# Performance work log

Hardware: AMD Instinct MI355X
Metric: run time of the kernel (lower is better)

Reference implementation:

```python
import jax, jax.numpy as jnp
import numpy as np

B, Q, C, H, NSTEPS = 1024, 96, 16, 100, 100  # batch, q (MA order), channels, hidden, Euler steps


def setup_inputs() -> dict:
    key = jax.random.key(0)
    ks = jax.random.split(key, 6)
    s = 0.1  # weight init scale
    return {
        "series": jax.random.normal(ks[0], (B, Q, C), jnp.float32),
        "rand_error": jax.random.normal(ks[1], (B, 1, C), jnp.float32),
        "W1": jax.random.normal(ks[2], (H, Q + 2), jnp.float32) * s,
        "b1": jnp.zeros((H,), jnp.float32),
        "W2": jax.random.normal(ks[3], (H, H), jnp.float32) * s,
        "b2": jnp.zeros((H,), jnp.float32),
        "W3": jax.random.normal(ks[4], (Q + 1, H), jnp.float32) * s,
        "b3": jnp.zeros((Q + 1,), jnp.float32),
    }


def _mlp(x, t, W1, b1, W2, b2, W3, b3):
    # x: (B, Q+1, C), t: (B, 1, C)  -> cat along feature dim, permute to (B, C, Q+2)
    inp = jnp.concatenate([x, t], axis=1).transpose(0, 2, 1)
    h = jnp.tanh(inp @ W1.T + b1)
    h = jnp.tanh(h @ W2.T + b2)
    out = h @ W3.T + b3            # (B, C, Q+1)
    return out.transpose(0, 2, 1)  # (B, Q+1, C)


def reference(series, rand_error, W1, b1, W2, b2, W3, b3):
    # ma_forecast sampling path: noise = cat(series, rand_error) then Euler flow sampling
    noise = jnp.concatenate([series, rand_error], axis=1)  # (B, Q+1, C)
    dt = jnp.float32(1.0 / NSTEPS)

    def step(x, i):
        t = jnp.ones((x.shape[0], 1, x.shape[2]), x.dtype) * (i.astype(x.dtype) / NSTEPS)
        pred = _mlp(x, t, W1, b1, W2, b2, W3, b3)
        return x + (pred - noise) * dt, None

    x, _ = jax.lax.scan(step, noise, jnp.arange(NSTEPS))
    return x
```

## Files before the change

### kernel.cpp

```cpp
#include <hip/hip_runtime.h>


#define NB 1024
#define NQ 96
#define NC 16
#define NH 100
#define QP1 97
#define QP2 98
#define NTHR 256
#define STR 136
#define NSTEPS_ 100
#define MT_K 128

typedef __attribute__((ext_vector_type(8))) short bf16x8;
typedef __attribute__((ext_vector_type(4))) short shortx4;
typedef __attribute__((ext_vector_type(4))) float f32x4;
typedef __attribute__((ext_vector_type(2))) float f32x2;
typedef __attribute__((ext_vector_type(4))) unsigned uintx4;

#define LO2(v) __builtin_shufflevector(v, v, 0, 1)
#define HI2(v) __builtin_shufflevector(v, v, 2, 3)

__device__ __forceinline__ f32x4 splat4(float f) {
  f32x4 v = f;
  return v;
}

__device__ __forceinline__ f32x2 splat2(float f) {
  f32x2 v = f;
  return v;
}

__device__ __forceinline__ short f2bf_rne(float f) {
  unsigned u = __builtin_bit_cast(unsigned, f);
  u = u + 0x7fffu + ((u >> 16) & 1u);
  return (short)(u >> 16);
}

__device__ __forceinline__ unsigned cvtpk_bf16(float a, float b) {
  unsigned r;
  asm("v_cvt_pk_bf16_f32 %0, %1, %2" : "=v"(r) : "v"(a), "v"(b));
  return r;
}

#if __has_builtin(__builtin_amdgcn_exp2f)
__device__ __forceinline__ float hexp2(float x) {
  return __builtin_amdgcn_exp2f(x);
}
#else
__device__ __forceinline__ float hexp2(float x) {
  float r;
  asm("v_exp_f32 %0, %1\n\ts_nop 1" : "=v"(r) : "v"(x));
  return r;
}
#endif

__device__ __forceinline__ float tanh1(float x) {
  float t = hexp2(x * 2.885390081777927f);
  float r = __builtin_amdgcn_rcpf(t + 1.0f);
  return fmaf(-2.0f, r, 1.0f);
}

__device__ __forceinline__ void tanh_pair(f32x2& p, f32x2& q) {
  p[0] = tanh1(p[0]);
  p[1] = tanh1(p[1]);
  q[0] = tanh1(q[0]);
  q[1] = tanh1(q[1]);
}

__global__ void __launch_bounds__(512) arima_prep(
    const float* __restrict__ W1, const float* __restrict__ b1,
    const float* __restrict__ W3, const float* __restrict__ b3,
    short* __restrict__ Mt, float* __restrict__ sv) {
  __shared__ float part[4][128];
  __shared__ float pb[128];
  const int n = blockIdx.x;
  const int tid = threadIdx.x;
  const int k = tid & 127, js = tid >> 7;
  float s = 0.0f;
  if (n < NH && k < NH) {
    int j0 = js * 25, j1 = (js == 3) ? QP1 : j0 + 25;
    for (int j = j0; j < j1; ++j)
      s = fmaf(W1[n * QP2 + j], W3[j * NH + k], s);
  }
  part[js][k] = s;
  if (tid < 128)
    pb[tid] = (tid < QP1 && n < NH) ? W1[n * QP2 + tid] * b3[tid] : 0.0f;
  __syncthreads();
  if (js == 0) {
    float tot = part[0][k] + part[1][k] + part[2][k] + part[3][k];
    Mt[n * MT_K + k] = f2bf_rne(0.01f * tot);
  }
  if (tid == 0) {
    float d = 0.0f;
    for (int j = 0; j < 128; ++j) d += pb[j];
    sv[n] = (n < NH) ? 0.01f * (d + b1[n] + W1[n * QP2 + QP1]) : 0.0f;
  }
}

__device__ void load_afrag(const float* __restrict__ W,
                           const float* __restrict__ bias, int ws, int mvalid,
                           int KW, int m, int quad, bf16x8 dst[4]) {
#pragma unroll
  for (int kb = 0; kb < 4; ++kb) {
    bf16x8 v;
#pragma unroll
    for (int i = 0; i < 8; ++i) {
      int kcol = kb * 32 + ((i >> 2) << 4) + quad * 4 + (i & 3);
      float f = 0.0f;
      if (m < mvalid) {
        if (kcol < KW) f = W[m * ws + kcol];
        else if (kcol == KW) f = bias[m];
      }
      v[i] = f2bf_rne(f);
    }
    dst[kb] = v;
  }
}

__device__ __forceinline__ void gemm_acc(const short* __restrict__ src,
                                         int rbase, const bf16x8 (&A)[2][4],
                                         f32x4 (&acc)[2]) {
#pragma unroll
  for (int kb = 0; kb < 4; ++kb) {
    bf16x8 bv = *(const bf16x8*)(src + rbase + kb * 32);
    acc[0] = __builtin_amdgcn_mfma_f32_16x16x32_bf16(A[0][kb], bv, acc[0], 0, 0, 0);
    acc[1] = __builtin_amdgcn_mfma_f32_16x16x32_bf16(A[1][kb], bv, acc[1], 0, 0, 0);
  }
}

__device__ __forceinline__ void write_tile(short* __restrict__ dst, int wrow,
                                           int T0, int quad, f32x2 a0,
                                           f32x2 a1, f32x2 b0, f32x2 b1) {
  uintx4 u;
  u.x = cvtpk_bf16(a0[0], a0[1]);
  u.y = cvtpk_bf16(a1[0], a1[1]);
  u.z = cvtpk_bf16(b0[0], b0[1]);
  u.w = cvtpk_bf16(b1[0], b1[1]);
  *(uintx4*)(dst + wrow + (T0 >> 1) * 32 + quad * 8) = u;
}

__global__ void __launch_bounds__(NTHR, 4)
arima_r20(const float* __restrict__ series,
          const float* __restrict__ rand_error, const float* __restrict__ W1,
          const float* __restrict__ b1, const float* __restrict__ W2,
          const float* __restrict__ b2, const float* __restrict__ W3,
          const float* __restrict__ b3, const short* __restrict__ Mt,
          const float* __restrict__ sv, float* __restrict__ out) {
  __shared__ __align__(16) short buf1[16 * STR];
  __shared__ __align__(16) short buf2[16 * STR];

  const int tid = threadIdx.x;
  const int w = tid >> 6, l = tid & 63;
  const int col = l & 15, quad = l >> 4;
  const int b = blockIdx.x;
  const int T0 = 2 * w;
  const int wrow = col * STR;
  const int rbase = wrow + quad * 8;
  const bool fixw = (w == 3 && quad == 1);

  {
    f32x4 xv[2];
#pragma unroll
    for (int t = 0; t < 2; ++t)
#pragma unroll
      for (int r = 0; r < 4; ++r) {
        int q = (T0 + t) * 16 + quad * 4 + r;
        float f = 0.0f;
        if (q < NQ) f = series[(b * NQ + q) * NC + col];
        else if (q == NQ) f = rand_error[b * NC + col];
        else if (q == QP2) f = 1.0f;
        xv[t][r] = f;
      }
    write_tile(buf2, wrow, T0, quad, LO2(xv[0]), HI2(xv[0]), LO2(xv[1]),
               HI2(xv[1]));
  }
  __syncthreads();

  f32x4 z[2], v[2];
  {
    bf16x8 a1[2][4];
#pragma unroll
    for (int t = 0; t < 2; ++t)
      load_afrag(W1, b1, QP2, NH, QP2, (T0 + t) * 16 + col, quad, a1[t]);
    z[0] = splat4(0.0f);
    z[1] = splat4(0.0f);
    gemm_acc(buf2, rbase, a1, z);
#pragma unroll
    for (int t = 0; t < 2; ++t) {
      f32x4 s;
#pragma unroll
      for (int r = 0; r < 4; ++r) s[r] = sv[(T0 + t) * 16 + quad * 4 + r];
      v[t] = s - splat4(0.01f) * z[t];
    }
  }
  {
    f32x2 p0 = LO2(z[0]), p1 = HI2(z[0]), p2 = LO2(z[1]), p3 = HI2(z[1]);
    tanh_pair(p0, p1);
    tanh_pair(p2, p3);
    if (fixw) p0[0] = 1.0f;
    write_tile(buf1, wrow, T0, quad, p0, p1, p2, p3);
  }
  __syncthreads();

  bf16x8 a2[2][4], am[2][4];
#pragma unroll
  for (int t = 0; t < 2; ++t) {
    load_afrag(W2, b2, NH, NH, NH, (T0 + t) * 16 + col, quad, a2[t]);
    const short* mrow = Mt + ((T0 + t) * 16 + col) * MT_K;
#pragma unroll
    for (int kb = 0; kb < 4; ++kb) {
      shortx4 lo = *(const shortx4*)(mrow + kb * 32 + quad * 4);
      shortx4 hi = *(const shortx4*)(mrow + kb * 32 + 16 + quad * 4);
      bf16x8 vv;
      vv[0] = lo[0]; vv[1] = lo[1]; vv[2] = lo[2]; vv[3] = lo[3];
      vv[4] = hi[0]; vv[5] = hi[1]; vv[6] = hi[2]; vv[7] = hi[3];
      am[t][kb] = vv;
    }
  }
  f32x2 h2s[2][2];
  h2s[0][0] = splat2(0.0f);
  h2s[0][1] = splat2(0.0f);
  h2s[1][0] = splat2(0.0f);
  h2s[1][1] = splat2(0.0f);

#pragma unroll 1
  for (int step = 0; step < NSTEPS_; ++step) {
    f32x4 acc[2];
    acc[0] = splat4(0.0f);
    acc[1] = splat4(0.0f);
    gemm_acc(buf1, rbase, a2, acc);
    {
      f32x2 p0 = LO2(acc[0]), p1 = HI2(acc[0]), p2 = LO2(acc[1]),
            p3 = HI2(acc[1]);
      tanh_pair(p0, p1);
      tanh_pair(p2, p3);
      write_tile(buf2, wrow, T0, quad, p0, p1, p2, p3);
      h2s[0][0] = h2s[0][0] + p0;
      h2s[0][1] = h2s[0][1] + p1;
      h2s[1][0] = h2s[1][0] + p2;
      h2s[1][1] = h2s[1][1] + p3;
    }
    __syncthreads();
    gemm_acc(buf2, rbase, am, z);
    {
      z[0] = z[0] + v[0];
      z[1] = z[1] + v[1];
      f32x2 q0 = LO2(z[0]), q1 = HI2(z[0]), q2 = LO2(z[1]), q3 = HI2(z[1]);
      tanh_pair(q0, q1);
      tanh_pair(q2, q3);
      if (fixw) q0[0] = 1.0f;
      write_tile(buf1, wrow, T0, quad, q0, q1, q2, q3);
    }
    __syncthreads();
  }

  {
    f32x2 ha00 = splat2(0.01f) * h2s[0][0];
    f32x2 ha01 = splat2(0.01f) * h2s[0][1];
    f32x2 ha10 = splat2(0.01f) * h2s[1][0];
    f32x2 ha11 = splat2(0.01f) * h2s[1][1];
    if (fixw) ha00[0] = 1.0f;
    write_tile(buf2, wrow, T0, quad, ha00, ha01, ha10, ha11);
  }
  __syncthreads();
  {
    bf16x8 a3[2][4];
#pragma unroll
    for (int t = 0; t < 2; ++t)
      load_afrag(W3, b3, NH, QP1, NH, (T0 + t) * 16 + col, quad, a3[t]);
    f32x4 o[2];
    o[0] = splat4(0.0f);
    o[1] = splat4(0.0f);
    gemm_acc(buf2, rbase, a3, o);
#pragma unroll
    for (int t = 0; t < 2; ++t)
#pragma unroll
      for (int r = 0; r < 4; ++r) {
        int q = (T0 + t) * 16 + quad * 4 + r;
        if (q < QP1) out[(b * QP1 + q) * NC + col] = o[t][r];
      }
  }
}

extern "C" void kernel_launch(void* const* d_in, const int* in_sizes, int n_in,
                              void* d_out, int out_size, void* d_ws,
                              size_t ws_size, hipStream_t stream) {
  const float* series = (const float*)d_in[0];
  const float* rand_error = (const float*)d_in[1];
  const float* W1 = (const float*)d_in[2];
  const float* b1 = (const float*)d_in[3];
  const float* W2 = (const float*)d_in[4];
  const float* b2 = (const float*)d_in[5];
  const float* W3 = (const float*)d_in[6];
  const float* b3 = (const float*)d_in[7];
  float* out = (float*)d_out;

  short* Mt = (short*)d_ws;
  float* sv = (float*)((char*)d_ws + MT_K * MT_K * 2);

  hipLaunchKernelGGL(arima_prep, dim3(128), dim3(512), 0, stream, W1, b1, W3,
                     b3, Mt, sv);
  hipLaunchKernelGGL(arima_r20, dim3(NB), dim3(NTHR), 0, stream, series,
                     rand_error, W1, b1, W2, b2, W3, b3, Mt, sv, out);
}
```

Baseline: 240.8 us.

## Pre-scale weights by tanh constant and issue own-slice MFMA before barrier

Folds the 2/ln2 tanh exponent constant into W1, W2, Mt and sv, so each tanh skips one multiply. Each wave now starts its GEMM with the k-block it just produced, taken straight from registers before the barrier, and reads the other three k-blocks from LDS after it in rotated order. The aim is to shorten the serial critical path through each step's barrier and spread LDS bank access across waves. The W2 and Mt fragments are also loaded before the first barrier. Scaling the weights before bf16 rounding slightly changes the rounding error.

Result: slower. 266.8 us (+10.8%).

```diff
diff --git a/kernel.cpp b/kernel.cpp
--- a/kernel.cpp
+++ b/kernel.cpp
@@ -11,6 +11,7 @@
 #define STR 136
 #define NSTEPS_ 100
 #define MT_K 128
+#define CC 2.885390081777927f
 
 typedef __attribute__((ext_vector_type(8))) short bf16x8;
 typedef __attribute__((ext_vector_type(4))) short shortx4;
@@ -55,17 +56,17 @@
 }
 #endif
 
-__device__ __forceinline__ float tanh1(float x) {
-  float t = hexp2(x * 2.885390081777927f);
+__device__ __forceinline__ float tanh1c(float x) {
+  float t = hexp2(x);
   float r = __builtin_amdgcn_rcpf(t + 1.0f);
   return fmaf(-2.0f, r, 1.0f);
 }
 
 __device__ __forceinline__ void tanh_pair(f32x2& p, f32x2& q) {
-  p[0] = tanh1(p[0]);
-  p[1] = tanh1(p[1]);
-  q[0] = tanh1(q[0]);
-  q[1] = tanh1(q[1]);
+  p[0] = tanh1c(p[0]);
+  p[1] = tanh1c(p[1]);
+  q[0] = tanh1c(q[0]);
+  q[1] = tanh1c(q[1]);
 }
 
 __global__ void __launch_bounds__(512) arima_prep(
@@ -89,33 +90,50 @@
   __syncthreads();
   if (js == 0) {
     float tot = part[0][k] + part[1][k] + part[2][k] + part[3][k];
-    Mt[n * MT_K + k] = f2bf_rne(0.01f * tot);
+    Mt[n * MT_K + k] = f2bf_rne(0.01f * CC * tot);
   }
   if (tid == 0) {
     float d = 0.0f;
     for (int j = 0; j < 128; ++j) d += pb[j];
-    sv[n] = (n < NH) ? 0.01f * (d + b1[n] + W1[n * QP2 + QP1]) : 0.0f;
-  }
+    sv[n] = (n < NH) ? 0.01f * CC * (d + b1[n] + W1[n * QP2 + QP1]) : 0.0f;
+  }
+}
+
+__device__ bf16x8 load_afrag_one(const float* __restrict__ W,
+                                 const float* __restrict__ bias, int ws,
+                                 int mvalid, int KW, int m, int quad, int kb,
+                                 float scale) {
+  bf16x8 v;
+#pragma unroll
+  for (int i = 0; i < 8; ++i) {
+    int kcol = kb * 32 + ((i >> 2) << 4) + quad * 4 + (i & 3);
+    float f = 0.0f;
+    if (m < mvalid) {
+      if (kcol < KW) f = W[m * ws + kcol];
+      else if (kcol == KW) f = bias[m];
+    }
+    v[i] = f2bf_rne(f * scale);
+  }
+  return v;
 }
 
 __device__ void load_afrag(const float* __restrict__ W,
                            const float* __restrict__ bias, int ws, int mvalid,
-                           int KW, int m, int quad, bf16x8 dst[4]) {
-#pragma unroll
-  for (int kb = 0; kb < 4; ++kb) {
-    bf16x8 v;
-#pragma unroll
-    for (int i = 0; i < 8; ++i) {
-      int kcol = kb * 32 + ((i >> 2) << 4) + quad * 4 + (i & 3);
-      float f = 0.0f;
-      if (m < mvalid) {
-        if (kcol < KW) f = W[m * ws + kcol];
-        else if (kcol == KW) f = bias[m];
-      }
-      v[i] = f2bf_rne(f);
-    }
-    dst[kb] = v;
-  }
+                           int KW, int m, int quad, float scale,
+                           bf16x8 dst[4]) {
+#pragma unroll
+  for (int kb = 0; kb < 4; ++kb)
+    dst[kb] = load_afrag_one(W, bias, ws, mvalid, KW, m, quad, kb, scale);
+}
+
+__device__ __forceinline__ bf16x8 mt_frag(const short* __restrict__ mrow,
+                                          int quad, int kb) {
+  shortx4 lo = *(const shortx4*)(mrow + kb * 32 + quad * 4);
+  shortx4 hi = *(const shortx4*)(mrow + kb * 32 + 16 + quad * 4);
+  bf16x8 vv;
+  vv[0] = lo[0]; vv[1] = lo[1]; vv[2] = lo[2]; vv[3] = lo[3];
+  vv[4] = hi[0]; vv[5] = hi[1]; vv[6] = hi[2]; vv[7] = hi[3];
+  return vv;
 }
 
 __device__ __forceinline__ void gemm_acc(const short* __restrict__ src,
@@ -129,19 +147,42 @@
   }
 }
 
-__device__ __forceinline__ void write_tile(short* __restrict__ dst, int wrow,
-                                           int T0, int quad, f32x2 a0,
-                                           f32x2 a1, f32x2 b0, f32x2 b1) {
+__device__ __forceinline__ void gemm_rest3(const short* __restrict__ src,
+                                           int o1, int o2, int o3,
+                                           const bf16x8 (&A)[2][4],
+                                           f32x4 (&acc)[2]) {
+  bf16x8 b1v = *(const bf16x8*)(src + o1);
+  acc[0] = __builtin_amdgcn_mfma_f32_16x16x32_bf16(A[0][1], b1v, acc[0], 0, 0, 0);
+  acc[1] = __builtin_amdgcn_mfma_f32_16x16x32_bf16(A[1][1], b1v, acc[1], 0, 0, 0);
+  bf16x8 b2v = *(const bf16x8*)(src + o2);
+  acc[0] = __builtin_amdgcn_mfma_f32_16x16x32_bf16(A[0][2], b2v, acc[0], 0, 0, 0);
+  acc[1] = __builtin_amdgcn_mfma_f32_16x16x32_bf16(A[1][2], b2v, acc[1], 0, 0, 0);
+  bf16x8 b3v = *(const bf16x8*)(src + o3);
+  acc[0] = __builtin_amdgcn_mfma_f32_16x16x32_bf16(A[0][3], b3v, acc[0], 0, 0, 0);
+  acc[1] = __builtin_amdgcn_mfma_f32_16x16x32_bf16(A[1][3], b3v, acc[1], 0, 0, 0);
+}
+
+__device__ __forceinline__ void gemm_own(const bf16x8& A0, const bf16x8& A1,
+                                         uintx4 u, f32x4 (&acc)[2]) {
+  bf16x8 bv = __builtin_bit_cast(bf16x8, u);
+  acc[0] = __builtin_amdgcn_mfma_f32_16x16x32_bf16(A0, bv, acc[0], 0, 0, 0);
+  acc[1] = __builtin_amdgcn_mfma_f32_16x16x32_bf16(A1, bv, acc[1], 0, 0, 0);
+}
+
+__device__ __forceinline__ uintx4 write_tile(short* __restrict__ dst, int wrow,
+                                             int T0, int quad, f32x2 a0,
+                                             f32x2 a1, f32x2 b0, f32x2 b1) {
   uintx4 u;
   u.x = cvtpk_bf16(a0[0], a0[1]);
   u.y = cvtpk_bf16(a1[0], a1[1]);
   u.z = cvtpk_bf16(b0[0], b0[1]);
   u.w = cvtpk_bf16(b1[0], b1[1]);
   *(uintx4*)(dst + wrow + (T0 >> 1) * 32 + quad * 8) = u;
+  return u;
 }
 
 __global__ void __launch_bounds__(NTHR, 4)
-arima_r20(const float* __restrict__ series,
+arima_r22(const float* __restrict__ series,
           const float* __restrict__ rand_error, const float* __restrict__ W1,
           const float* __restrict__ b1, const float* __restrict__ W2,
           const float* __restrict__ b2, const float* __restrict__ W3,
@@ -158,6 +199,9 @@
   const int wrow = col * STR;
   const int rbase = wrow + quad * 8;
   const bool fixw = (w == 3 && quad == 1);
+  const int o1 = rbase + ((w + 1) & 3) * 32;
+  const int o2 = rbase + ((w + 2) & 3) * 32;
+  const int o3 = rbase + ((w + 3) & 3) * 32;
 
   {
     f32x4 xv[2];
@@ -175,6 +219,19 @@
     write_tile(buf2, wrow, T0, quad, LO2(xv[0]), HI2(xv[0]), LO2(xv[1]),
                HI2(xv[1]));
   }
+
+  bf16x8 a2r[2][4], amr[2][4];
+#pragma unroll
+  for (int t = 0; t < 2; ++t) {
+    const int m = (T0 + t) * 16 + col;
+    const short* mrow = Mt + m * MT_K;
+#pragma unroll
+    for (int j = 0; j < 4; ++j) {
+      const int kbv = (w + j) & 3;
+      a2r[t][j] = load_afrag_one(W2, b2, NH, NH, NH, m, quad, kbv, CC);
+      amr[t][j] = mt_frag(mrow, quad, kbv);
+    }
+  }
   __syncthreads();
 
   f32x4 z[2], v[2];
@@ -182,7 +239,7 @@
     bf16x8 a1[2][4];
 #pragma unroll
     for (int t = 0; t < 2; ++t)
-      load_afrag(W1, b1, QP2, NH, QP2, (T0 + t) * 16 + col, quad, a1[t]);
+      load_afrag(W1, b1, QP2, NH, QP2, (T0 + t) * 16 + col, quad, CC, a1[t]);
     z[0] = splat4(0.0f);
     z[1] = splat4(0.0f);
     gemm_acc(buf2, rbase, a1, z);
@@ -194,30 +251,19 @@
       v[t] = s - splat4(0.01f) * z[t];
     }
   }
+  f32x4 acc[2];
   {
     f32x2 p0 = LO2(z[0]), p1 = HI2(z[0]), p2 = LO2(z[1]), p3 = HI2(z[1]);
     tanh_pair(p0, p1);
     tanh_pair(p2, p3);
     if (fixw) p0[0] = 1.0f;
-    write_tile(buf1, wrow, T0, quad, p0, p1, p2, p3);
+    uintx4 hu1 = write_tile(buf1, wrow, T0, quad, p0, p1, p2, p3);
+    acc[0] = splat4(0.0f);
+    acc[1] = splat4(0.0f);
+    gemm_own(a2r[0][0], a2r[1][0], hu1, acc);
   }
   __syncthreads();
 
-  bf16x8 a2[2][4], am[2][4];
-#pragma unroll
-  for (int t = 0; t < 2; ++t) {
-    load_afrag(W2, b2, NH, NH, NH, (T0 + t) * 16 + col, quad, a2[t]);
-    const short* mrow = Mt + ((T0 + t) * 16 + col) * MT_K;
-#pragma unroll
-    for (int kb = 0; kb < 4; ++kb) {
-      shortx4 lo = *(const shortx4*)(mrow + kb * 32 + quad * 4);
-      shortx4 hi = *(const shortx4*)(mrow + kb * 32 + 16 + quad * 4);
-      bf16x8 vv;
-      vv[0] = lo[0]; vv[1] = lo[1]; vv[2] = lo[2]; vv[3] = lo[3];
-      vv[4] = hi[0]; vv[5] = hi[1]; vv[6] = hi[2]; vv[7] = hi[3];
-      am[t][kb] = vv;
-    }
-  }
   f32x2 h2s[2][2];
   h2s[0][0] = splat2(0.0f);
   h2s[0][1] = splat2(0.0f);
@@ -226,23 +272,21 @@
 
 #pragma unroll 1
   for (int step = 0; step < NSTEPS_; ++step) {
-    f32x4 acc[2];
-    acc[0] = splat4(0.0f);
-    acc[1] = splat4(0.0f);
-    gemm_acc(buf1, rbase, a2, acc);
+    gemm_rest3(buf1, o1, o2, o3, a2r, acc);
     {
       f32x2 p0 = LO2(acc[0]), p1 = HI2(acc[0]), p2 = LO2(acc[1]),
             p3 = HI2(acc[1]);
       tanh_pair(p0, p1);
       tanh_pair(p2, p3);
-      write_tile(buf2, wrow, T0, quad, p0, p1, p2, p3);
+      uintx4 hu2 = write_tile(buf2, wrow, T0, quad, p0, p1, p2, p3);
       h2s[0][0] = h2s[0][0] + p0;
       h2s[0][1] = h2s[0][1] + p1;
       h2s[1][0] = h2s[1][0] + p2;
       h2s[1][1] = h2s[1][1] + p3;
+      gemm_own(amr[0][0], amr[1][0], hu2, z);
     }
     __syncthreads();
-    gemm_acc(buf2, rbase, am, z);
+    gemm_rest3(buf2, o1, o2, o3, amr, z);
     {
       z[0] = z[0] + v[0];
       z[1] = z[1] + v[1];
@@ -250,7 +294,10 @@
       tanh_pair(q0, q1);
       tanh_pair(q2, q3);
       if (fixw) q0[0] = 1.0f;
-      write_tile(buf1, wrow, T0, quad, q0, q1, q2, q3);
+      uintx4 hu1 = write_tile(buf1, wrow, T0, quad, q0, q1, q2, q3);
+      acc[0] = splat4(0.0f);
+      acc[1] = splat4(0.0f);
+      gemm_own(a2r[0][0], a2r[1][0], hu1, acc);
     }
     __syncthreads();
   }
@@ -268,7 +315,7 @@
     bf16x8 a3[2][4];
 #pragma unroll
     for (int t = 0; t < 2; ++t)
-      load_afrag(W3, b3, NH, QP1, NH, (T0 + t) * 16 + col, quad, a3[t]);
+      load_afrag(W3, b3, NH, QP1, NH, (T0 + t) * 16 + col, quad, 1.0f, a3[t]);
     f32x4 o[2];
     o[0] = splat4(0.0f);
     o[1] = splat4(0.0f);
@@ -301,6 +348,6 @@
 
   hipLaunchKernelGGL(arima_prep, dim3(128), dim3(512), 0, stream, W1, b1, W3,
                      b3, Mt, sv);
-  hipLaunchKernelGGL(arima_r20, dim3(NB), dim3(NTHR), 0, stream, series,
+  hipLaunchKernelGGL(arima_r22, dim3(NB), dim3(NTHR), 0, stream, series,
                      rand_error, W1, b1, W2, b2, W3, b3, Mt, sv, out);
 }
```
